# Kernel optimization log

Hardware: AMD Instinct MI355X
Metric: run time of the kernel (lower is better)

Reference implementation:

```python
import jax, jax.numpy as jnp
import numpy as np

NUM_TOKENS = 16384
HIDDEN = 2048
NUM_EXPERTS = 64
TOP_K = 2


def setup_inputs() -> dict:
    key = jax.random.key(0)
    kx, kw = jax.random.split(key)
    x = jax.random.normal(kx, (NUM_TOKENS, HIDDEN), dtype=jnp.float32)
    # nn.Linear weight is (num_experts, hidden); store transposed for x @ W
    W_gate = jax.random.normal(kw, (HIDDEN, NUM_EXPERTS), dtype=jnp.float32) * (1.0 / np.sqrt(HIDDEN))
    return {"x": x, "W_gate": W_gate}


def reference(x, W_gate):
    # gate matmul + softmax over experts
    logits = jnp.einsum("th,he->te", x, W_gate)          # (T, E)
    probs = jax.nn.softmax(logits, axis=-1)
    # top-k selection and renormalization
    top_k_weights, top_k_indices = jax.lax.top_k(probs, TOP_K)  # (T, k), (T, k)
    top_k_weights = top_k_weights / (jnp.sum(top_k_weights, axis=-1, keepdims=True) + 1e-9)
    # Switch-style load-balancing aux loss using top-1 assignments
    num_tokens = x.shape[0]
    top1 = top_k_indices[:, 0]
    tokens_per_expert = jnp.zeros((NUM_EXPERTS,), dtype=probs.dtype).at[top1].add(1.0)
    f = tokens_per_expert / num_tokens                    # fraction of tokens per expert
    P = jnp.mean(probs, axis=0)                           # mean router prob per expert
    aux_loss = NUM_EXPERTS * jnp.sum(f * P)
    return (top_k_weights, top_k_indices, aux_loss)
```

## Files before the change

kernel.cpp:

```cpp
#include <hip/hip_runtime.h>
#include <math.h>

#define NUM_TOKENS 16384
#define HIDDEN 2048
#define NUM_EXPERTS 64
#define TOPK 2

#define TM 64
#define KH 64
#define XS_STR 68

#define IDX_OFF 32768
#define AUX_OFF 65536

__global__ __launch_bounds__(256) void router_kernel(
    const float* __restrict__ x, const float* __restrict__ Wg,
    float* __restrict__ out, float* __restrict__ ws)
{
    __shared__ float sA[TM * XS_STR];
    __shared__ float sB[KH * NUM_EXPERTS];

    const int tid = threadIdx.x;
    const int bid = blockIdx.x;
    const int tx = tid & 15;
    const int ty = tid >> 4;
    const int tokBase = bid * TM;

    float C[4][4] = {{0.f,0.f,0.f,0.f},{0.f,0.f,0.f,0.f},{0.f,0.f,0.f,0.f},{0.f,0.f,0.f,0.f}};

    for (int hb = 0; hb < HIDDEN; hb += KH) {
        #pragma unroll
        for (int p = 0; p < 4; ++p) {
            int li = p * 256 + tid;
            int t  = li >> 4;
            int hq = li & 15;
            float4 v = *reinterpret_cast<const float4*>(
                &x[(size_t)(tokBase + t) * HIDDEN + hb + hq * 4]);
            *reinterpret_cast<float4*>(&sA[t * XS_STR + hq * 4]) = v;
        }
        #pragma unroll
        for (int p = 0; p < 4; ++p) {
            int li = p * 256 + tid;
            float4 v = *reinterpret_cast<const float4*>(
                &Wg[(size_t)hb * NUM_EXPERTS + li * 4]);
            *reinterpret_cast<float4*>(&sB[li * 4]) = v;
        }
        __syncthreads();

        #pragma unroll
        for (int k4 = 0; k4 < KH / 4; ++k4) {
            float xa[4][4];
            float wa[4][4];
            #pragma unroll
            for (int i = 0; i < 4; ++i) {
                float4 v = *reinterpret_cast<const float4*>(
                    &sA[(ty * 4 + i) * XS_STR + k4 * 4]);
                xa[i][0] = v.x; xa[i][1] = v.y; xa[i][2] = v.z; xa[i][3] = v.w;
            }
            #pragma unroll
            for (int kk = 0; kk < 4; ++kk) {
                float4 v = *reinterpret_cast<const float4*>(
                    &sB[(k4 * 4 + kk) * NUM_EXPERTS + tx * 4]);
                wa[kk][0] = v.x; wa[kk][1] = v.y; wa[kk][2] = v.z; wa[kk][3] = v.w;
            }
            #pragma unroll
            for (int i = 0; i < 4; ++i)
                #pragma unroll
                for (int kk = 0; kk < 4; ++kk)
                    #pragma unroll
                    for (int jj = 0; jj < 4; ++jj)
                        C[i][jj] = fmaf(xa[i][kk], wa[kk][jj], C[i][jj]);
        }
        __syncthreads();
    }

    #pragma unroll
    for (int i = 0; i < 4; ++i) {
        float4 v; v.x = C[i][0]; v.y = C[i][1]; v.z = C[i][2]; v.w = C[i][3];
        *reinterpret_cast<float4*>(&sA[(ty * 4 + i) * XS_STR + tx * 4]) = v;
    }
    __syncthreads();

    const int wave = tid >> 6;
    const int lane = tid & 63;
    float accP = 0.f;
    float accC = 0.f;

    for (int tt = 0; tt < TM / 4; ++tt) {
        int t = wave * (TM / 4) + tt;
        float l = sA[t * XS_STR + lane];

        float m = l;
        #pragma unroll
        for (int off = 32; off >= 1; off >>= 1) m = fmaxf(m, __shfl_xor(m, off));
        float p = expf(l - m);
        float Z = p;
        #pragma unroll
        for (int off = 32; off >= 1; off >>= 1) Z += __shfl_xor(Z, off);
        float prob = p / Z;

        float v1 = prob; int i1 = lane;
        #pragma unroll
        for (int off = 32; off >= 1; off >>= 1) {
            float ov = __shfl_xor(v1, off);
            int   oi = __shfl_xor(i1, off);
            if (ov > v1 || (ov == v1 && oi < i1)) { v1 = ov; i1 = oi; }
        }
        float v2 = (lane == i1) ? -1.f : prob; int i2 = lane;
        #pragma unroll
        for (int off = 32; off >= 1; off >>= 1) {
            float ov = __shfl_xor(v2, off);
            int   oi = __shfl_xor(i2, off);
            if (ov > v2 || (ov == v2 && oi < i2)) { v2 = ov; i2 = oi; }
        }

        accP += prob;
        if (lane == i1) accC += 1.f;

        if (lane == 0) {
            float s = v1 + v2 + 1e-9f;
            size_t o = (size_t)(tokBase + t) * 2;
            out[o]               = v1 / s;
            out[o + 1]           = v2 / s;
            out[IDX_OFF + o]     = (float)i1;
            out[IDX_OFF + o + 1] = (float)i2;
        }
    }

    sB[wave * 64 + lane]       = accP;
    sB[256 + wave * 64 + lane] = accC;
    __syncthreads();
    if (tid < 64) {
        float sp = sB[tid] + sB[64 + tid] + sB[128 + tid] + sB[192 + tid];
        float sc = sB[256 + tid] + sB[320 + tid] + sB[384 + tid] + sB[448 + tid];
        ws[(size_t)bid * 128 + tid]      = sp;
        ws[(size_t)bid * 128 + 64 + tid] = sc;
    }
}

__global__ __launch_bounds__(64) void finalize_kernel(
    const float* __restrict__ ws, float* __restrict__ out)
{
    int e = threadIdx.x;
    float sp = 0.f, sc = 0.f;
    for (int b = 0; b < NUM_TOKENS / TM; ++b) {
        sp += ws[(size_t)b * 128 + e];
        sc += ws[(size_t)b * 128 + 64 + e];
    }
    float val = (sc * (1.0f / NUM_TOKENS)) * (sp * (1.0f / NUM_TOKENS));
    #pragma unroll
    for (int off = 32; off >= 1; off >>= 1) val += __shfl_xor(val, off);
    if (e == 0) out[AUX_OFF] = (float)NUM_EXPERTS * val;
}

extern "C" void kernel_launch(void* const* d_in, const int* in_sizes, int n_in,
                              void* d_out, int out_size, void* d_ws, size_t ws_size,
                              hipStream_t stream) {
    const float* x  = (const float*)d_in[0];
    const float* Wg = (const float*)d_in[1];
    float* out = (float*)d_out;
    float* ws  = (float*)d_ws;

    router_kernel<<<NUM_TOKENS / TM, 256, 0, stream>>>(x, Wg, out, ws);
    finalize_kernel<<<1, 64, 0, stream>>>(ws, out);
}
```

Before: 116.6 us.

## Rewrite router GEMM as register-only wave-per-8-tokens with software prefetch

Replaces the LDS-tiled 64x64 GEMM with a scheme where each wave owns 8 tokens and each lane one expert. It streams x as float4 broadcasts and W columns from global memory through double-buffered registers, with no shared-memory staging or barriers in the main loop. It adds dummy prefetch loads, summed into a workspace slot, to pull x lines into cache ahead of use, and launches 512 blocks with occupancy hints. This aims to cut LDS traffic and syncs and raise parallelism, at the cost of redundant global/L2 reads of W per wave and extra prefetch load instructions.

Measured after the change: 389.3 us. 234% more time.

```diff
diff --git a/kernel.cpp b/kernel.cpp
--- a/kernel.cpp
+++ b/kernel.cpp
@@ -4,146 +4,148 @@
 #define NUM_TOKENS 16384
 #define HIDDEN 2048
 #define NUM_EXPERTS 64
-#define TOPK 2
-
-#define TM 64
-#define KH 64
-#define XS_STR 68
 
 #define IDX_OFF 32768
 #define AUX_OFF 65536
 
-__global__ __launch_bounds__(256) void router_kernel(
+#define TPW 8
+#define WPB 4
+#define TPB (TPW * WPB)
+#define NBLK (NUM_TOKENS / TPB)
+#define PF_DIST 256
+#define WS_DUMMY (NBLK * 128)
+
+__global__ __launch_bounds__(256, 2) void router_kernel(
     const float* __restrict__ x, const float* __restrict__ Wg,
     float* __restrict__ out, float* __restrict__ ws)
 {
-    __shared__ float sA[TM * XS_STR];
-    __shared__ float sB[KH * NUM_EXPERTS];
+    __shared__ float sP[WPB][NUM_EXPERTS];
+    __shared__ float sC[WPB][NUM_EXPERTS];
 
-    const int tid = threadIdx.x;
-    const int bid = blockIdx.x;
-    const int tx = tid & 15;
-    const int ty = tid >> 4;
-    const int tokBase = bid * TM;
+    const int tid  = threadIdx.x;
+    const int wid  = __builtin_amdgcn_readfirstlane(tid >> 6);
+    const int lane = tid & 63;
+    const int tok0 = blockIdx.x * TPB + wid * TPW;
+    const float* __restrict__ xb = x + (size_t)tok0 * HIDDEN;
 
-    float C[4][4] = {{0.f,0.f,0.f,0.f},{0.f,0.f,0.f,0.f},{0.f,0.f,0.f,0.f},{0.f,0.f,0.f,0.f}};
+    float C[TPW];
+    #pragma unroll
+    for (int t = 0; t < TPW; ++t) C[t] = 0.f;
 
-    for (int hb = 0; hb < HIDDEN; hb += KH) {
+    float  w4[4][4];
+    float4 xbuf[2][TPW];
+    float  pfv[8];
+    float  pfw[8];
+    float  pf_acc = 0.f;
+
+    #pragma unroll
+    for (int r = 0; r < TPW; ++r) pfw[r] = xb[(size_t)r * HIDDEN + (lane << 2)];
+    #pragma unroll
+    for (int j = 0; j < 8; ++j) pfv[j] = 0.f;
+    #pragma unroll
+    for (int t = 0; t < TPW; ++t)
+        xbuf[0][t] = *reinterpret_cast<const float4*>(xb + (size_t)t * HIDDEN);
+    #pragma unroll
+    for (int j = 0; j < 2; ++j)
         #pragma unroll
-        for (int p = 0; p < 4; ++p) {
-            int li = p * 256 + tid;
-            int t  = li >> 4;
-            int hq = li & 15;
-            float4 v = *reinterpret_cast<const float4*>(
-                &x[(size_t)(tokBase + t) * HIDDEN + hb + hq * 4]);
-            *reinterpret_cast<float4*>(&sA[t * XS_STR + hq * 4]) = v;
+        for (int q = 0; q < 4; ++q)
+            w4[j][q] = Wg[(size_t)(j * 4 + q) * NUM_EXPERTS + lane];
+
+    for (int kb = 0; kb < HIDDEN; kb += 32) {
+        #pragma unroll
+        for (int j = 0; j < 8; ++j) {
+            const int k = kb + j * 4;
+            {
+                const int kn  = k + 4;
+                const int knn = (kn == HIDDEN) ? 0 : kn;
+                #pragma unroll
+                for (int t = 0; t < TPW; ++t)
+                    xbuf[(j + 1) & 1][t] =
+                        *reinterpret_cast<const float4*>(xb + (size_t)t * HIDDEN + knn);
+            }
+            {
+                const int kw = (k + 8) & (HIDDEN - 1);
+                #pragma unroll
+                for (int q = 0; q < 4; ++q)
+                    w4[(j + 2) & 3][q] = Wg[(size_t)(kw + q) * NUM_EXPERTS + lane];
+            }
+            pf_acc += pfv[j];
+            if (kb + PF_DIST < HIDDEN)
+                pfv[j] = xb[(size_t)j * HIDDEN + (kb + PF_DIST) + (lane & 31)];
+            #pragma unroll
+            for (int q = 0; q < 4; ++q)
+                #pragma unroll
+                for (int t = 0; t < TPW; ++t)
+                    C[t] = fmaf(reinterpret_cast<const float*>(&xbuf[j & 1][t])[q],
+                                w4[j & 3][q], C[t]);
         }
-        #pragma unroll
-        for (int p = 0; p < 4; ++p) {
-            int li = p * 256 + tid;
-            float4 v = *reinterpret_cast<const float4*>(
-                &Wg[(size_t)hb * NUM_EXPERTS + li * 4]);
-            *reinterpret_cast<float4*>(&sB[li * 4]) = v;
-        }
-        __syncthreads();
-
-        #pragma unroll
-        for (int k4 = 0; k4 < KH / 4; ++k4) {
-            float xa[4][4];
-            float wa[4][4];
-            #pragma unroll
-            for (int i = 0; i < 4; ++i) {
-                float4 v = *reinterpret_cast<const float4*>(
-                    &sA[(ty * 4 + i) * XS_STR + k4 * 4]);
-                xa[i][0] = v.x; xa[i][1] = v.y; xa[i][2] = v.z; xa[i][3] = v.w;
-            }
-            #pragma unroll
-            for (int kk = 0; kk < 4; ++kk) {
-                float4 v = *reinterpret_cast<const float4*>(
-                    &sB[(k4 * 4 + kk) * NUM_EXPERTS + tx * 4]);
-                wa[kk][0] = v.x; wa[kk][1] = v.y; wa[kk][2] = v.z; wa[kk][3] = v.w;
-            }
-            #pragma unroll
-            for (int i = 0; i < 4; ++i)
-                #pragma unroll
-                for (int kk = 0; kk < 4; ++kk)
-                    #pragma unroll
-                    for (int jj = 0; jj < 4; ++jj)
-                        C[i][jj] = fmaf(xa[i][kk], wa[kk][jj], C[i][jj]);
-        }
-        __syncthreads();
     }
 
     #pragma unroll
-    for (int i = 0; i < 4; ++i) {
-        float4 v; v.x = C[i][0]; v.y = C[i][1]; v.z = C[i][2]; v.w = C[i][3];
-        *reinterpret_cast<float4*>(&sA[(ty * 4 + i) * XS_STR + tx * 4]) = v;
-    }
-    __syncthreads();
+    for (int j = 0; j < 8; ++j) pf_acc += pfv[j];
+    #pragma unroll
+    for (int r = 0; r < TPW; ++r) pf_acc += pfw[r];
 
-    const int wave = tid >> 6;
-    const int lane = tid & 63;
-    float accP = 0.f;
-    float accC = 0.f;
-
-    for (int tt = 0; tt < TM / 4; ++tt) {
-        int t = wave * (TM / 4) + tt;
-        float l = sA[t * XS_STR + lane];
-
+    float accP = 0.f, accC = 0.f;
+    #pragma unroll
+    for (int t = 0; t < TPW; ++t) {
+        const float l = C[t];
         float m = l;
         #pragma unroll
         for (int off = 32; off >= 1; off >>= 1) m = fmaxf(m, __shfl_xor(m, off));
-        float p = expf(l - m);
+        const float p = expf(l - m);
         float Z = p;
         #pragma unroll
         for (int off = 32; off >= 1; off >>= 1) Z += __shfl_xor(Z, off);
-        float prob = p / Z;
+        const float prob = p / Z;
 
         float v1 = prob; int i1 = lane;
         #pragma unroll
         for (int off = 32; off >= 1; off >>= 1) {
-            float ov = __shfl_xor(v1, off);
-            int   oi = __shfl_xor(i1, off);
+            const float ov = __shfl_xor(v1, off);
+            const int   oi = __shfl_xor(i1, off);
             if (ov > v1 || (ov == v1 && oi < i1)) { v1 = ov; i1 = oi; }
         }
         float v2 = (lane == i1) ? -1.f : prob; int i2 = lane;
         #pragma unroll
         for (int off = 32; off >= 1; off >>= 1) {
-            float ov = __shfl_xor(v2, off);
-            int   oi = __shfl_xor(i2, off);
+            const float ov = __shfl_xor(v2, off);
+            const int   oi = __shfl_xor(i2, off);
             if (ov > v2 || (ov == v2 && oi < i2)) { v2 = ov; i2 = oi; }
         }
 
         accP += prob;
-        if (lane == i1) accC += 1.f;
+        accC += (lane == i1) ? 1.f : 0.f;
 
         if (lane == 0) {
-            float s = v1 + v2 + 1e-9f;
-            size_t o = (size_t)(tokBase + t) * 2;
-            out[o]               = v1 / s;
-            out[o + 1]           = v2 / s;
-            out[IDX_OFF + o]     = (float)i1;
-            out[IDX_OFF + o + 1] = (float)i2;
+            const float s = v1 + v2 + 1e-9f;
+            const size_t o = (size_t)(tok0 + t) * 2;
+            float2 wo; wo.x = v1 / s; wo.y = v2 / s;
+            *reinterpret_cast<float2*>(&out[o]) = wo;
+            float2 io; io.x = (float)i1; io.y = (float)i2;
+            *reinterpret_cast<float2*>(&out[IDX_OFF + o]) = io;
         }
     }
 
-    sB[wave * 64 + lane]       = accP;
-    sB[256 + wave * 64 + lane] = accC;
+    sP[wid][lane] = accP;
+    sC[wid][lane] = accC;
     __syncthreads();
     if (tid < 64) {
-        float sp = sB[tid] + sB[64 + tid] + sB[128 + tid] + sB[192 + tid];
-        float sc = sB[256 + tid] + sB[320 + tid] + sB[384 + tid] + sB[448 + tid];
-        ws[(size_t)bid * 128 + tid]      = sp;
-        ws[(size_t)bid * 128 + 64 + tid] = sc;
+        const float sp = sP[0][tid] + sP[1][tid] + sP[2][tid] + sP[3][tid];
+        const float sc = sC[0][tid] + sC[1][tid] + sC[2][tid] + sC[3][tid];
+        ws[(size_t)blockIdx.x * 128 + tid]      = sp;
+        ws[(size_t)blockIdx.x * 128 + 64 + tid] = sc;
     }
+    if (lane == 0)
+        ws[WS_DUMMY + (size_t)blockIdx.x * WPB + wid] = pf_acc;
 }
 
 __global__ __launch_bounds__(64) void finalize_kernel(
     const float* __restrict__ ws, float* __restrict__ out)
 {
-    int e = threadIdx.x;
+    const int e = threadIdx.x;
     float sp = 0.f, sc = 0.f;
-    for (int b = 0; b < NUM_TOKENS / TM; ++b) {
+    for (int b = 0; b < NBLK; ++b) {
         sp += ws[(size_t)b * 128 + e];
         sc += ws[(size_t)b * 128 + 64 + e];
     }
@@ -161,6 +163,6 @@
     float* out = (float*)d_out;
     float* ws  = (float*)d_ws;
 
-    router_kernel<<<NUM_TOKENS / TM, 256, 0, stream>>>(x, Wg, out, ws);
+    router_kernel<<<NBLK, 256, 0, stream>>>(x, Wg, out, ws);
     finalize_kernel<<<1, 64, 0, stream>>>(ws, out);
 }
```
